# Performance work log

Measured on AMD Instinct MI355X. Metric: run time of the kernel, lower is better.

The kernel has to match this reference:

```python
import jax, jax.numpy as jnp
import numpy as np

EMBED = 768
HEADS = 12


def setup_inputs() -> dict:
    key = jax.random.key(0)
    k1, k2, k3 = jax.random.split(key, 3)
    B, N, E = 2, 2048, EMBED
    x = jax.random.normal(k1, (B, N, E), dtype=jnp.float32)
    w_qkv = jax.random.normal(k2, (3 * E, E), dtype=jnp.float32) * (1.0 / np.sqrt(E))
    b_qkv = jnp.zeros((3 * E,), dtype=jnp.float32)
    w_o = jax.random.normal(k3, (E, E), dtype=jnp.float32) * (1.0 / np.sqrt(E))
    b_o = jnp.zeros((E,), dtype=jnp.float32)
    return {"x": x, "w_qkv": w_qkv, "b_qkv": b_qkv, "w_o": w_o, "b_o": b_o}


def reference(x, w_qkv, b_qkv, w_o, b_o):
    B, N, E = x.shape
    H = HEADS
    d = E // H
    # fused qkv projection (torch Linear: x @ W^T + b)
    qkv = x @ w_qkv.T + b_qkv                       # [B, N, 3E]
    # Rearrange 'b n (h qkv e) -> b qkv h n e'
    qkv = qkv.reshape(B, N, H, 3, d).transpose(0, 3, 2, 1, 4)  # [B, 3, H, N, d]
    q, k, v = qkv[:, 0], qkv[:, 1], qkv[:, 2]       # each [B, H, N, d]
    scores = jnp.einsum("bhqd,bhkd->bhqk", q, k)    # [B, H, N, N]
    attn = jax.nn.softmax(scores / jnp.sqrt(jnp.float32(E)), axis=-1)
    ctx = jnp.einsum("bhqk,bhkd->bhqd", attn, v)    # [B, H, N, d]
    ctx = ctx.transpose(0, 2, 1, 3).reshape(B, N, E)  # 'b h n d -> b n (h d)'
    out = ctx @ w_o.T + b_o
    return out
```

## Files before the change

kernel.cpp:

```cpp
#include <hip/hip_runtime.h>

#define BB 2
#define NN 2048
#define EE 768
#define HH 12
#define DD 64
#define MM (BB*NN)
#define E3 (3*EE)
#define QSCALE 0.05205877280961602f

typedef __bf16 bf16x8 __attribute__((ext_vector_type(8)));
typedef float  f32x4  __attribute__((ext_vector_type(4)));
typedef unsigned short u16x8 __attribute__((ext_vector_type(8)));

#define MFMA(a,b,c) __builtin_amdgcn_mfma_f32_16x16x32_bf16(a,b,c,0,0,0)

__device__ __forceinline__ unsigned short f2bf(float f) {
    unsigned int u = __float_as_uint(f);
    u += 0x7FFFu + ((u >> 16) & 1u);
    return (unsigned short)(u >> 16);
}

typedef __attribute__((address_space(3))) unsigned int as3u32;
typedef __attribute__((address_space(1))) unsigned int as1u32;
__device__ __forceinline__ void gll16(const void* g, void* l) {
    __builtin_amdgcn_global_load_lds((const as1u32*)(uintptr_t)g,
                                     (as3u32*)(unsigned int)(uintptr_t)l, 16, 0, 0);
}

#define XB4 786432
#define WQ4 442368
#define WO4 147456
__global__ __launch_bounds__(256)
void cast3(const float* __restrict__ x, const float* __restrict__ wq,
           const float* __restrict__ wo, unsigned short* __restrict__ dst) {
    int i = blockIdx.x * 256 + threadIdx.x;
    const float* src;
    int off;
    if (i < XB4)            { src = x;  off = i; }
    else if (i < XB4+WQ4)   { src = wq; off = i - XB4; }
    else                    { src = wo; off = i - XB4 - WQ4; }
    float4 v = ((const float4*)src)[off];
    ushort4 o;
    o.x = f2bf(v.x); o.y = f2bf(v.y); o.z = f2bf(v.z); o.w = f2bf(v.w);
    ((ushort4*)dst)[i] = o;
}

__global__ __launch_bounds__(256)
void gemm_qkv(const unsigned short* __restrict__ A, const unsigned short* __restrict__ W,
              const float* __restrict__ bias,
              unsigned short* __restrict__ o0, unsigned short* __restrict__ o1,
              unsigned short* __restrict__ o2)
{
    __shared__ unsigned short As[128 * 32];
    __shared__ unsigned short Bs[64 * 32];

    const int tid = threadIdx.x;
    const int l = tid & 63;
    const int w = tid >> 6;
    const int m0 = blockIdx.x * 128;
    const int c0 = blockIdx.y * 64;
    const int wm = (w >> 1) * 64;
    const int wn = (w & 1) * 32;

    const unsigned short* s_src[3];
    unsigned short* s_dst[3];
    #pragma unroll
    for (int s = 0; s < 3; ++s) {
        const int ch = 3*w + s;
        if (ch < 8) {
            s_src[s] = A + (size_t)(m0 + ch*16 + (l>>2)) * EE + (l&3)*8;
            s_dst[s] = &As[ch*512];
        } else {
            s_src[s] = W + (size_t)(c0 + (ch-8)*16 + (l>>2)) * EE + (l&3)*8;
            s_dst[s] = &Bs[(ch-8)*512];
        }
    }

    const f32x4 zero4 = {0.f, 0.f, 0.f, 0.f};
    f32x4 acc[4][2];
    #pragma unroll
    for (int i = 0; i < 4; ++i)
        #pragma unroll
        for (int j = 0; j < 2; ++j) acc[i][j] = zero4;

    for (int k0 = 0; k0 < EE; k0 += 32) {
        __syncthreads();
        #pragma unroll
        for (int s = 0; s < 3; ++s) gll16(s_src[s] + k0, s_dst[s]);
        __syncthreads();

        bf16x8 af[4], bf[2];
        #pragma unroll
        for (int i = 0; i < 4; ++i)
            af[i] = *(const bf16x8*)&As[(wm + 16*i + (l&15))*32 + (l>>4)*8];
        #pragma unroll
        for (int j = 0; j < 2; ++j)
            bf[j] = *(const bf16x8*)&Bs[(wn + 16*j + (l&15))*32 + (l>>4)*8];
        #pragma unroll
        for (int i = 0; i < 4; ++i)
            #pragma unroll
            for (int j = 0; j < 2; ++j)
                acc[i][j] = MFMA(af[i], bf[j], acc[i][j]);
    }

    const int sec = c0 >> 6;
    const int hh = sec / 3;
    const int tt = sec - hh*3;
    #pragma unroll
    for (int j = 0; j < 2; ++j) {
        const int col = c0 + wn + 16*j + (l&15);
        const int dcol = wn + 16*j + (l&15);
        const float bj = bias[col];
        #pragma unroll
        for (int i = 0; i < 4; ++i) {
            const int row0 = m0 + wm + 16*i + (l>>4)*4;
            const int b = row0 >> 11;
            const int n = row0 & (NN - 1);
            if (tt == 2) {
                ushort4 pk;
                pk.x = f2bf(acc[i][j][0] + bj);
                pk.y = f2bf(acc[i][j][1] + bj);
                pk.z = f2bf(acc[i][j][2] + bj);
                pk.w = f2bf(acc[i][j][3] + bj);
                *(ushort4*)&o2[(((size_t)b*HH + hh)*DD + dcol)*NN + n] = pk;
            } else {
                unsigned short* dst = (tt == 0) ? o0 : o1;
                #pragma unroll
                for (int r = 0; r < 4; ++r) {
                    float val = acc[i][j][r] + bj;
                    if (tt == 0) val *= QSCALE;
                    dst[(((size_t)b*HH + hh)*NN + n + r)*DD + dcol] = f2bf(val);
                }
            }
        }
    }
}

__global__ __launch_bounds__(256)
void gemm_out(const unsigned short* __restrict__ A, const unsigned short* __restrict__ W,
              const float* __restrict__ bias, float* __restrict__ of)
{
    __shared__ unsigned short As[64 * 32];
    __shared__ unsigned short Bs[64 * 32];

    const int tid = threadIdx.x;
    const int l = tid & 63;
    const int w = tid >> 6;
    const int m0 = blockIdx.x * 64;
    const int c0 = blockIdx.y * 64;
    const int wm = (w >> 1) * 32;
    const int wn = (w & 1) * 32;

    const unsigned short* s_src[2];
    unsigned short* s_dst[2];
    #pragma unroll
    for (int s = 0; s < 2; ++s) {
        const int ch = 2*w + s;
        if (ch < 4) {
            s_src[s] = A + (size_t)(m0 + ch*16 + (l>>2)) * EE + (l&3)*8;
            s_dst[s] = &As[ch*512];
        } else {
            s_src[s] = W + (size_t)(c0 + (ch-4)*16 + (l>>2)) * EE + (l&3)*8;
            s_dst[s] = &Bs[(ch-4)*512];
        }
    }

    const f32x4 zero4 = {0.f, 0.f, 0.f, 0.f};
    f32x4 acc[2][2];
    #pragma unroll
    for (int i = 0; i < 2; ++i)
        #pragma unroll
        for (int j = 0; j < 2; ++j) acc[i][j] = zero4;

    for (int k0 = 0; k0 < EE; k0 += 32) {
        __syncthreads();
        #pragma unroll
        for (int s = 0; s < 2; ++s) gll16(s_src[s] + k0, s_dst[s]);
        __syncthreads();

        bf16x8 af[2], bf[2];
        #pragma unroll
        for (int i = 0; i < 2; ++i)
            af[i] = *(const bf16x8*)&As[(wm + 16*i + (l&15))*32 + (l>>4)*8];
        #pragma unroll
        for (int j = 0; j < 2; ++j)
            bf[j] = *(const bf16x8*)&Bs[(wn + 16*j + (l&15))*32 + (l>>4)*8];
        #pragma unroll
        for (int i = 0; i < 2; ++i)
            #pragma unroll
            for (int j = 0; j < 2; ++j)
                acc[i][j] = MFMA(af[i], bf[j], acc[i][j]);
    }

    #pragma unroll
    for (int j = 0; j < 2; ++j) {
        const int col = c0 + wn + 16*j + (l&15);
        const float bj = bias[col];
        #pragma unroll
        for (int i = 0; i < 2; ++i) {
            #pragma unroll
            for (int r = 0; r < 4; ++r) {
                const int row = m0 + wm + 16*i + (l>>4)*4 + r;
                of[(size_t)row * EE + col] = acc[i][j][r] + bj;
            }
        }
    }
}

struct KVT { u16x8 k0, k1, k2, k3, v0, v1, v2, v3; };

__global__ __launch_bounds__(256)
void attn_mfma(const unsigned short* __restrict__ Q, const unsigned short* __restrict__ K,
               const unsigned short* __restrict__ Vt_g, unsigned short* __restrict__ ctx)
{
    __shared__ unsigned short Ks[2 * 64 * 64];
    __shared__ unsigned short Vt[2 * 64 * 64];
    __shared__ unsigned short Pq[4 * 2 * 16 * 64];

    const int tid = threadIdx.x;
    const int l = tid & 63;
    const int w = tid >> 6;
    const int quad = l >> 4;
    const int lc = l & 15;
    const int x7 = lc & 7;

    const int id = blockIdx.x;
    const int bh = id % 24;
    const int bq = id / 24;
    const int b  = bh / 12;
    const int h  = bh - b*12;
    const size_t hb = (size_t)bh * NN * DD;

    const f32x4 zero4 = {0.f, 0.f, 0.f, 0.f};

    const int qrow = bq*64 + w*16 + lc;
    const bf16x8 qf0 = *(const bf16x8*)(Q + hb + (size_t)qrow*DD +      quad*8);
    const bf16x8 qf1 = *(const bf16x8*)(Q + hb + (size_t)qrow*DD + 32 + quad*8);

    f32x4 o[4];
    #pragma unroll
    for (int dj = 0; dj < 4; ++dj) o[dj] = zero4;
    float lsum = 0.f;

    const int srow = tid >> 2;
    const int sc = tid & 3;
    const unsigned short* kbase = K + hb + (size_t)srow*DD + sc*16;
    const unsigned short* vbase = Vt_g + hb + (size_t)srow*NN + sc*16;
    const int c0s = ((2*sc)     ^ (srow & 7)) * 8;
    const int c1s = ((2*sc + 1) ^ (srow & 7)) * 8;
    const int so = srow * 64;

    const int chq0 = ((    quad) ^ x7) * 8;
    const int chq1 = ((4 + quad) ^ x7) * 8;
    const int pw = w * 2048;
    const int prd0 = lc*64 + (((    2*quad) ^ (lc & 14)) * 4);
    const int prd1 = lc*64 + (((8 + 2*quad) ^ (lc & 14)) * 4);

    auto loadt = [&](KVT& R, int kt) {
        const unsigned short* k0p = kbase + (size_t)kt*128*DD;
        const unsigned short* v0p = vbase + kt*128;
        R.k0 = *(const u16x8*)k0p;
        R.k1 = *(const u16x8*)(k0p + 8);
        R.k2 = *(const u16x8*)(k0p + (size_t)64*DD);
        R.k3 = *(const u16x8*)(k0p + (size_t)64*DD + 8);
        R.v0 = *(const u16x8*)v0p;
        R.v1 = *(const u16x8*)(v0p + 8);
        R.v2 = *(const u16x8*)(v0p + 64);
        R.v3 = *(const u16x8*)(v0p + 64 + 8);
    };

    auto step = [&](KVT& CUR, KVT& NXT, int kt) {
        asm volatile("s_waitcnt lgkmcnt(0)" ::: "memory");
        __builtin_amdgcn_s_barrier();

        *(u16x8*)&Ks[so + c0s]        = CUR.k0;
        *(u16x8*)&Ks[so + c1s]        = CUR.k1;
        *(u16x8*)&Ks[4096 + so + c0s] = CUR.k2;
        *(u16x8*)&Ks[4096 + so + c1s] = CUR.k3;
        *(u16x8*)&Vt[so + c0s]        = CUR.v0;
        *(u16x8*)&Vt[so + c1s]        = CUR.v1;
        *(u16x8*)&Vt[4096 + so + c0s] = CUR.v2;
        *(u16x8*)&Vt[4096 + so + c1s] = CUR.v3;

        if (kt + 1 < NN/128) loadt(NXT, kt + 1);

        asm volatile("s_waitcnt lgkmcnt(0)" ::: "memory");
        __builtin_amdgcn_s_barrier();
        __builtin_amdgcn_sched_barrier(0);

        #pragma unroll
        for (int hf = 0; hf < 2; ++hf) {
            const int base = hf * 4096;
            const int pb = pw + hf * 1024;

            f32x4 st[4];
            #pragma unroll
            for (int jf = 0; jf < 4; ++jf) {
                bf16x8 kf0 = *(const bf16x8*)&Ks[base + (16*jf + lc)*64 + chq0];
                bf16x8 kf1 = *(const bf16x8*)&Ks[base + (16*jf + lc)*64 + chq1];
                f32x4 acc0 = MFMA(kf0, qf0, zero4);
                st[jf] = MFMA(kf1, qf1, acc0);
            }

            #pragma unroll
            for (int jf = 0; jf < 4; ++jf) {
                float e0 = __builtin_amdgcn_exp2f(st[jf][0]);
                float e1 = __builtin_amdgcn_exp2f(st[jf][1]);
                float e2 = __builtin_amdgcn_exp2f(st[jf][2]);
                float e3 = __builtin_amdgcn_exp2f(st[jf][3]);
                lsum += (e0 + e1) + (e2 + e3);
                ushort4 pk;
                pk.x = f2bf(e0); pk.y = f2bf(e1); pk.z = f2bf(e2); pk.w = f2bf(e3);
                *(ushort4*)&Pq[pb + lc*64 + (((4*jf + quad) ^ (lc & 14)) * 4)] = pk;
            }

            bf16x8 pf0 = *(const bf16x8*)&Pq[pb + prd0];
            bf16x8 pf1 = *(const bf16x8*)&Pq[pb + prd1];
            #pragma unroll
            for (int dj = 0; dj < 4; ++dj) {
                bf16x8 vf0 = *(const bf16x8*)&Vt[base + (16*dj + lc)*64 + chq0];
                bf16x8 vf1 = *(const bf16x8*)&Vt[base + (16*dj + lc)*64 + chq1];
                o[dj] = MFMA(vf0, pf0, o[dj]);
                o[dj] = MFMA(vf1, pf1, o[dj]);
            }
        }
    };

    KVT ra, rb;
    loadt(ra, 0);
    for (int it = 0; it < NN/256; ++it) {
        step(ra, rb, 2*it);
        step(rb, ra, 2*it + 1);
    }

    lsum += __shfl_xor(lsum, 16);
    lsum += __shfl_xor(lsum, 32);
    const float inv = 1.f / lsum;

    const int n = bq*64 + w*16 + lc;
    #pragma unroll
    for (int dj = 0; dj < 4; ++dj) {
        ushort4 pk;
        pk.x = f2bf(o[dj][0] * inv);
        pk.y = f2bf(o[dj][1] * inv);
        pk.z = f2bf(o[dj][2] * inv);
        pk.w = f2bf(o[dj][3] * inv);
        *(ushort4*)&ctx[((size_t)(b*NN + n))*EE + h*DD + 16*dj + quad*4] = pk;
    }
}

extern "C" void kernel_launch(void* const* d_in, const int* in_sizes, int n_in,
                              void* d_out, int out_size, void* d_ws, size_t ws_size,
                              hipStream_t stream)
{
    const float* x     = (const float*)d_in[0];
    const float* w_qkv = (const float*)d_in[1];
    const float* b_qkv = (const float*)d_in[2];
    const float* w_o   = (const float*)d_in[3];
    const float* b_o   = (const float*)d_in[4];
    float* out = (float*)d_out;

    unsigned short* wsu = (unsigned short*)d_ws;
    const size_t XB = (size_t)MM * EE;
    const size_t WQ = (size_t)E3 * EE;
    const size_t WO = (size_t)EE * EE;
    const size_t HS = (size_t)BB * HH * NN * DD;
    unsigned short* xb   = wsu;
    unsigned short* wqb  = xb  + XB;
    unsigned short* wob  = wqb + WQ;
    unsigned short* qb   = wob + WO;
    unsigned short* kb   = qb  + HS;
    unsigned short* vtb  = kb  + HS;
    unsigned short* ctxb = vtb + HS;

    cast3<<<(XB4 + WQ4 + WO4)/256, 256, 0, stream>>>(x, w_qkv, w_o, xb);

    dim3 g1(MM/128, E3/64);
    gemm_qkv<<<g1, 256, 0, stream>>>(xb, wqb, b_qkv, qb, kb, vtb);

    attn_mfma<<<768, 256, 0, stream>>>(qb, kb, vtb, ctxb);

    dim3 g3(MM/64, EE/64);
    gemm_out<<<g3, 256, 0, stream>>>(ctxb, wob, b_o, out);
}
```

Measured before the change: 170.1 us.

## Keep softmax probabilities in registers by permuting V key order

Removes the per-warp LDS round-trip for the P matrix. The exponentiated scores stay in registers and are packed directly into MFMA operand fragments. To make that register layout line up with the PV MFMA's k dimension, the V^T tile's key columns are loaded and shuffled into a permuted order when staged to shared memory. This cuts LDS writes and reads plus the shared buffer, at the cost of some extra shuffle instructions and a tighter layout dependence.

New measurement: 168.5 us. Within noise of the previous version (-0.9%).

```diff
diff --git a/kernel.cpp b/kernel.cpp
--- a/kernel.cpp
+++ b/kernel.cpp
@@ -19,6 +19,10 @@
     unsigned int u = __float_as_uint(f);
     u += 0x7FFFu + ((u >> 16) & 1u);
     return (unsigned short)(u >> 16);
+}
+
+__device__ __forceinline__ bf16x8 as_bf16x8(u16x8 v) {
+    union { u16x8 u; bf16x8 b; } c; c.u = v; return c.b;
 }
 
 typedef __attribute__((address_space(3))) unsigned int as3u32;
@@ -216,7 +220,6 @@
 {
     __shared__ unsigned short Ks[2 * 64 * 64];
     __shared__ unsigned short Vt[2 * 64 * 64];
-    __shared__ unsigned short Pq[4 * 2 * 16 * 64];
 
     const int tid = threadIdx.x;
     const int l = tid & 63;
@@ -246,16 +249,14 @@
     const int srow = tid >> 2;
     const int sc = tid & 3;
     const unsigned short* kbase = K + hb + (size_t)srow*DD + sc*16;
-    const unsigned short* vbase = Vt_g + hb + (size_t)srow*NN + sc*16;
+    const int keyA = (sc & 1)*8 + (sc >> 1)*32;
+    const unsigned short* vbase = Vt_g + hb + (size_t)srow*NN + keyA;
     const int c0s = ((2*sc)     ^ (srow & 7)) * 8;
     const int c1s = ((2*sc + 1) ^ (srow & 7)) * 8;
     const int so = srow * 64;
 
     const int chq0 = ((    quad) ^ x7) * 8;
     const int chq1 = ((4 + quad) ^ x7) * 8;
-    const int pw = w * 2048;
-    const int prd0 = lc*64 + (((    2*quad) ^ (lc & 14)) * 4);
-    const int prd1 = lc*64 + (((8 + 2*quad) ^ (lc & 14)) * 4);
 
     auto loadt = [&](KVT& R, int kt) {
         const unsigned short* k0p = kbase + (size_t)kt*128*DD;
@@ -265,23 +266,27 @@
         R.k2 = *(const u16x8*)(k0p + (size_t)64*DD);
         R.k3 = *(const u16x8*)(k0p + (size_t)64*DD + 8);
         R.v0 = *(const u16x8*)v0p;
-        R.v1 = *(const u16x8*)(v0p + 8);
+        R.v1 = *(const u16x8*)(v0p + 16);
         R.v2 = *(const u16x8*)(v0p + 64);
-        R.v3 = *(const u16x8*)(v0p + 64 + 8);
+        R.v3 = *(const u16x8*)(v0p + 64 + 16);
     };
 
     auto step = [&](KVT& CUR, KVT& NXT, int kt) {
         asm volatile("s_waitcnt lgkmcnt(0)" ::: "memory");
         __builtin_amdgcn_s_barrier();
 
+        u16x8 w0 = __builtin_shufflevector(CUR.v0, CUR.v1, 0,1,2,3, 8,9,10,11);
+        u16x8 w1 = __builtin_shufflevector(CUR.v0, CUR.v1, 4,5,6,7, 12,13,14,15);
+        u16x8 w2 = __builtin_shufflevector(CUR.v2, CUR.v3, 0,1,2,3, 8,9,10,11);
+        u16x8 w3 = __builtin_shufflevector(CUR.v2, CUR.v3, 4,5,6,7, 12,13,14,15);
         *(u16x8*)&Ks[so + c0s]        = CUR.k0;
         *(u16x8*)&Ks[so + c1s]        = CUR.k1;
         *(u16x8*)&Ks[4096 + so + c0s] = CUR.k2;
         *(u16x8*)&Ks[4096 + so + c1s] = CUR.k3;
-        *(u16x8*)&Vt[so + c0s]        = CUR.v0;
-        *(u16x8*)&Vt[so + c1s]        = CUR.v1;
-        *(u16x8*)&Vt[4096 + so + c0s] = CUR.v2;
-        *(u16x8*)&Vt[4096 + so + c1s] = CUR.v3;
+        *(u16x8*)&Vt[so + c0s]        = w0;
+        *(u16x8*)&Vt[so + c1s]        = w1;
+        *(u16x8*)&Vt[4096 + so + c0s] = w2;
+        *(u16x8*)&Vt[4096 + so + c1s] = w3;
 
         if (kt + 1 < NN/128) loadt(NXT, kt + 1);
 
@@ -292,7 +297,6 @@
         #pragma unroll
         for (int hf = 0; hf < 2; ++hf) {
             const int base = hf * 4096;
-            const int pb = pw + hf * 1024;
 
             f32x4 st[4];
             #pragma unroll
@@ -303,20 +307,26 @@
                 st[jf] = MFMA(kf1, qf1, acc0);
             }
 
+            f32x4 ev[4];
             #pragma unroll
             for (int jf = 0; jf < 4; ++jf) {
-                float e0 = __builtin_amdgcn_exp2f(st[jf][0]);
-                float e1 = __builtin_amdgcn_exp2f(st[jf][1]);
-                float e2 = __builtin_amdgcn_exp2f(st[jf][2]);
-                float e3 = __builtin_amdgcn_exp2f(st[jf][3]);
-                lsum += (e0 + e1) + (e2 + e3);
-                ushort4 pk;
-                pk.x = f2bf(e0); pk.y = f2bf(e1); pk.z = f2bf(e2); pk.w = f2bf(e3);
-                *(ushort4*)&Pq[pb + lc*64 + (((4*jf + quad) ^ (lc & 14)) * 4)] = pk;
-            }
-
-            bf16x8 pf0 = *(const bf16x8*)&Pq[pb + prd0];
-            bf16x8 pf1 = *(const bf16x8*)&Pq[pb + prd1];
+                ev[jf][0] = __builtin_amdgcn_exp2f(st[jf][0]);
+                ev[jf][1] = __builtin_amdgcn_exp2f(st[jf][1]);
+                ev[jf][2] = __builtin_amdgcn_exp2f(st[jf][2]);
+                ev[jf][3] = __builtin_amdgcn_exp2f(st[jf][3]);
+                lsum += (ev[jf][0] + ev[jf][1]) + (ev[jf][2] + ev[jf][3]);
+            }
+            u16x8 p0, p1;
+            #pragma unroll
+            for (int r = 0; r < 4; ++r) {
+                p0[r]     = f2bf(ev[0][r]);
+                p0[r + 4] = f2bf(ev[1][r]);
+                p1[r]     = f2bf(ev[2][r]);
+                p1[r + 4] = f2bf(ev[3][r]);
+            }
+            const bf16x8 pf0 = as_bf16x8(p0);
+            const bf16x8 pf1 = as_bf16x8(p1);
+
             #pragma unroll
             for (int dj = 0; dj < 4; ++dj) {
                 bf16x8 vf0 = *(const bf16x8*)&Vt[base + (16*dj + lc)*64 + chq0];
```
